# Optimization experiments

Measured on AMD Instinct MI355X. Metric: run time of the kernel, lower is better.

## Reference

```python
import jax, jax.numpy as jnp
import numpy as np

L, B, T, C, H, V, CTX = 4, 2, 1024, 1024, 16, 50257, 2048
D = C // H
EPS = 1e-5
NEG_SLOPE = 0.01


def layer_norm(x, w, b):
    mu = jnp.mean(x, axis=-1, keepdims=True)
    var = jnp.mean(jnp.square(x - mu), axis=-1, keepdims=True)
    return (x - mu) * jax.lax.rsqrt(var + EPS) * w + b


def setup_inputs() -> dict:
    key = jax.random.key(0)
    ks = jax.random.split(key, 8)
    s = 0.02  # init std as in _init_weights
    return {
        "idx": jax.random.randint(ks[0], (B, T), 0, V),
        "wte": jax.random.normal(ks[1], (V, C), jnp.float32) * s,
        "wpe": jax.random.normal(ks[2], (CTX, C), jnp.float32) * s,
        "ln1_w": jnp.ones((L, C), jnp.float32),
        "ln1_b": jnp.zeros((L, C), jnp.float32),
        "attn_w": jax.random.normal(ks[3], (L, C, 3 * C), jnp.float32) * s,
        "attn_b": jnp.zeros((L, 3 * C), jnp.float32),
        "proj_w": jax.random.normal(ks[4], (L, C, C), jnp.float32) * s,
        "proj_b": jnp.zeros((L, C), jnp.float32),
        "ln2_w": jnp.ones((L, C), jnp.float32),
        "ln2_b": jnp.zeros((L, C), jnp.float32),
        "fc_w": jax.random.normal(ks[5], (L, C, 4 * C), jnp.float32) * s,
        "fc_b": jnp.zeros((L, 4 * C), jnp.float32),
        "fcproj_w": jax.random.normal(ks[6], (L, 4 * C, C), jnp.float32) * s,
        "fcproj_b": jnp.zeros((L, C), jnp.float32),
        "lnf_w": jnp.ones((C,), jnp.float32),
        "lnf_b": jnp.zeros((C,), jnp.float32),
    }


def reference(idx, wte, wpe, ln1_w, ln1_b, attn_w, attn_b, proj_w, proj_b,
              ln2_w, ln2_b, fc_w, fc_b, fcproj_w, fcproj_b, lnf_w, lnf_b):
    t = idx.shape[1]
    x = wte[idx] + wpe[:t]  # [B,T,C]; dropout=0 => identity
    causal = jnp.tril(jnp.ones((t, t), bool))  # [T,T]
    scale = 1.0 / np.sqrt(D)
    for l in range(L):
        # --- causal self-attention ---
        h = layer_norm(x, ln1_w[l], ln1_b[l])
        qkv = h @ attn_w[l] + attn_b[l]  # [B,T,3C]
        q, k, v = jnp.split(qkv, 3, axis=-1)
        q = q.reshape(B, t, H, D)
        k = k.reshape(B, t, H, D)
        v = v.reshape(B, t, H, D)
        att = jnp.einsum('bthd,bshd->bhts', q, k) * scale  # [B,H,T,T]
        att = jnp.where(causal, att, -jnp.inf)
        att = jax.nn.softmax(att, axis=-1)
        y = jnp.einsum('bhts,bshd->bthd', att, v).reshape(B, t, C)
        x = x + y @ proj_w[l] + proj_b[l]
        # --- MLP ---
        h = layer_norm(x, ln2_w[l], ln2_b[l])
        h = h @ fc_w[l] + fc_b[l]
        h = jnp.where(h >= 0, h, NEG_SLOPE * h)  # LeakyReLU(0.01)
        x = x + h @ fcproj_w[l] + fcproj_b[l]
    x = layer_norm(x, lnf_w, lnf_b)
    # targets=None path: lm_head on last position only, tied weight = wte
    logits = x[:, -1:, :] @ wte.T  # [B,1,V]
    return logits
```

## Files before the change

### kernel.cpp

```cpp
#include <hip/hip_runtime.h>
#include <hip/hip_bf16.h>


#define TT 1024
#define CC 1024
#define NHEAD 16
#define DHEAD 64
#define NBATCH 2
#define VOCAB 50257

typedef __attribute__((ext_vector_type(8))) short bf16x8;
typedef __attribute__((ext_vector_type(4))) float f32x4;

#define GPTR(p) (const __attribute__((address_space(1))) void*)(p)
#define LPTR(p) (__attribute__((address_space(3))) void*)(p)

__device__ __forceinline__ unsigned short f2bf(float f) {
  union { float f; unsigned u; } v; v.f = f;
  unsigned r = v.u + 0x7fffu + ((v.u >> 16) & 1u);
  return (unsigned short)(r >> 16);
}
__device__ __forceinline__ float bf2f(unsigned short u) {
  union { unsigned u; float f; } v; v.u = ((unsigned)u) << 16;
  return v.f;
}

__device__ __forceinline__ f32x4 mfma_bf16(bf16x8 a, bf16x8 b, f32x4 c) {
  return __builtin_amdgcn_mfma_f32_16x16x32_bf16(a, b, c, 0, 0, 0);
}

__global__ __launch_bounds__(256) void embed_k(const int* __restrict__ idx,
    const float* __restrict__ wte, const float* __restrict__ wpe,
    float* __restrict__ x)
{
  int row = blockIdx.x;
  int t = row & (TT - 1);
  int tok = idx[row];
  const float4* a = (const float4*)(wte + (size_t)tok * CC);
  const float4* p = (const float4*)(wpe + (size_t)t * CC);
  float4* o = (float4*)(x + (size_t)row * CC);
  int i = threadIdx.x;
  float4 va = a[i], vp = p[i];
  o[i] = make_float4(va.x + vp.x, va.y + vp.y, va.z + vp.z, va.w + vp.w);
}

__device__ __forceinline__ unsigned pk2(float lo, float hi) {
  return (unsigned)f2bf(lo) | ((unsigned)f2bf(hi) << 16);
}

__global__ __launch_bounds__(256) void ln_k(const float* __restrict__ x,
    const float* __restrict__ w, const float* __restrict__ b,
    unsigned short* __restrict__ out)
{
  int row = blockIdx.x * 4 + (threadIdx.x >> 6);
  int lane = threadIdx.x & 63;
  const float* xr = x + (size_t)row * CC + lane * 16;
  float4 v[4];
  float s = 0.f, ss = 0.f;
#pragma unroll
  for (int i = 0; i < 4; ++i) {
    v[i] = *(const float4*)(xr + i * 4);
    s  += v[i].x + v[i].y + v[i].z + v[i].w;
    ss += v[i].x*v[i].x + v[i].y*v[i].y + v[i].z*v[i].z + v[i].w*v[i].w;
  }
#pragma unroll
  for (int off = 1; off < 64; off <<= 1) {
    s  += __shfl_xor(s, off, 64);
    ss += __shfl_xor(ss, off, 64);
  }
  float mu = s * (1.f / CC);
  float var = ss * (1.f / CC) - mu * mu;
  float rstd = rsqrtf(var + 1e-5f);
  const float* wr = w + lane * 16;
  const float* br = b + lane * 16;
  unsigned q[8];
#pragma unroll
  for (int i = 0; i < 4; ++i) {
    float4 wv = *(const float4*)(wr + i * 4);
    float4 bv = *(const float4*)(br + i * 4);
    float o0 = (v[i].x - mu) * rstd * wv.x + bv.x;
    float o1 = (v[i].y - mu) * rstd * wv.y + bv.y;
    float o2 = (v[i].z - mu) * rstd * wv.z + bv.z;
    float o3 = (v[i].w - mu) * rstd * wv.w + bv.w;
    q[i*2+0] = pk2(o0, o1);
    q[i*2+1] = pk2(o2, o3);
  }
  uint4* op = (uint4*)(out + (size_t)row * CC + lane * 16);
  op[0] = make_uint4(q[0], q[1], q[2], q[3]);
  op[1] = make_uint4(q[4], q[5], q[6], q[7]);
}

__global__ __launch_bounds__(256) void redln_k(float* __restrict__ x,
    const float* __restrict__ P, const float* __restrict__ bias,
    const float* __restrict__ lw, const float* __restrict__ lb,
    unsigned short* __restrict__ out, int splits)
{
  int row = blockIdx.x * 4 + (threadIdx.x >> 6);
  int lane = threadIdx.x & 63;
  const int c0 = lane * 16;
  float* xw = x + (size_t)row * CC + c0;
  float4 v[4];
#pragma unroll
  for (int i = 0; i < 4; ++i) v[i] = *(const float4*)(xw + i * 4);
  {
    const float4* b4 = (const float4*)(bias + c0);
#pragma unroll
    for (int i = 0; i < 4; ++i) {
      float4 bv = b4[i];
      v[i].x += bv.x; v[i].y += bv.y; v[i].z += bv.z; v[i].w += bv.w;
    }
  }
  for (int sp = 0; sp < splits; ++sp) {
    const float4* p4 = (const float4*)(P + ((size_t)sp * 2048 + row) * CC + c0);
#pragma unroll
    for (int i = 0; i < 4; ++i) {
      float4 pv = p4[i];
      v[i].x += pv.x; v[i].y += pv.y; v[i].z += pv.z; v[i].w += pv.w;
    }
  }
  float s = 0.f, ss = 0.f;
#pragma unroll
  for (int i = 0; i < 4; ++i) {
    *(float4*)(xw + i * 4) = v[i];
    s  += v[i].x + v[i].y + v[i].z + v[i].w;
    ss += v[i].x*v[i].x + v[i].y*v[i].y + v[i].z*v[i].z + v[i].w*v[i].w;
  }
#pragma unroll
  for (int off = 1; off < 64; off <<= 1) {
    s  += __shfl_xor(s, off, 64);
    ss += __shfl_xor(ss, off, 64);
  }
  float mu = s * (1.f / CC);
  float var = ss * (1.f / CC) - mu * mu;
  float rstd = rsqrtf(var + 1e-5f);
  const float* wr = lw + c0;
  const float* br = lb + c0;
  unsigned q[8];
#pragma unroll
  for (int i = 0; i < 4; ++i) {
    float4 wv = *(const float4*)(wr + i * 4);
    float4 bv = *(const float4*)(br + i * 4);
    float o0 = (v[i].x - mu) * rstd * wv.x + bv.x;
    float o1 = (v[i].y - mu) * rstd * wv.y + bv.y;
    float o2 = (v[i].z - mu) * rstd * wv.z + bv.z;
    float o3 = (v[i].w - mu) * rstd * wv.w + bv.w;
    q[i*2+0] = pk2(o0, o1);
    q[i*2+1] = pk2(o2, o3);
  }
  uint4* op = (uint4*)(out + (size_t)row * CC + c0);
  op[0] = make_uint4(q[0], q[1], q[2], q[3]);
  op[1] = make_uint4(q[4], q[5], q[6], q[7]);
}

__global__ void lnrow_k(const float* __restrict__ x,
    const float* __restrict__ w, const float* __restrict__ b,
    float* __restrict__ outv)
{
  int row = blockIdx.x;
  int lane = threadIdx.x;
  const float* xr = x + ((size_t)(row * TT + (TT - 1))) * CC + lane * 16;
  float4 v[4];
  float s = 0.f, ss = 0.f;
#pragma unroll
  for (int i = 0; i < 4; ++i) {
    v[i] = *(const float4*)(xr + i * 4);
    s  += v[i].x + v[i].y + v[i].z + v[i].w;
    ss += v[i].x*v[i].x + v[i].y*v[i].y + v[i].z*v[i].z + v[i].w*v[i].w;
  }
#pragma unroll
  for (int off = 1; off < 64; off <<= 1) {
    s  += __shfl_xor(s, off, 64);
    ss += __shfl_xor(ss, off, 64);
  }
  float mu = s * (1.f / CC);
  float var = ss * (1.f / CC) - mu * mu;
  float rstd = rsqrtf(var + 1e-5f);
  float* op = outv + (size_t)row * CC + lane * 16;
  const float* wr = w + lane * 16;
  const float* br = b + lane * 16;
#pragma unroll
  for (int i = 0; i < 4; ++i) {
    float4 wv = *(const float4*)(wr + i * 4);
    float4 bv = *(const float4*)(br + i * 4);
    float4 o;
    o.x = (v[i].x - mu) * rstd * wv.x + bv.x;
    o.y = (v[i].y - mu) * rstd * wv.y + bv.y;
    o.z = (v[i].z - mu) * rstd * wv.z + bv.z;
    o.w = (v[i].w - mu) * rstd * wv.w + bv.w;
    *(float4*)(op + i * 4) = o;
  }
}

__global__ __launch_bounds__(256) void wconv_k(const float* __restrict__ W,
    unsigned short* __restrict__ Wt, int K, int N)
{
  const size_t lo = (size_t)blockIdx.z * K * N;
  __shared__ float tile[64][65];
  const int k0 = blockIdx.x << 6;
  const int n0 = blockIdx.y << 6;
  const int t = threadIdx.x;
  {
    const int r = t >> 4, c4 = t & 15;
#pragma unroll
    for (int p = 0; p < 4; ++p) {
      int kr = r + (p << 4);
      float4 v = *(const float4*)(W + lo + (size_t)(k0 + kr) * N + n0 + (c4 << 2));
      tile[kr][(c4 << 2) + 0] = v.x;
      tile[kr][(c4 << 2) + 1] = v.y;
      tile[kr][(c4 << 2) + 2] = v.z;
      tile[kr][(c4 << 2) + 3] = v.w;
    }
  }
  __syncthreads();
  {
    const int n = t >> 2, kq = t & 3;
    bf16x8 o0, o1;
#pragma unroll
    for (int e = 0; e < 8; ++e) o0[e] = (short)f2bf(tile[(kq << 4) + e][n]);
#pragma unroll
    for (int e = 0; e < 8; ++e) o1[e] = (short)f2bf(tile[(kq << 4) + 8 + e][n]);
    unsigned short* dst = Wt + lo + (size_t)(n0 + n) * K + k0 + (kq << 4);
    *(bf16x8*)dst = o0;
    *(bf16x8*)(dst + 8) = o1;
  }
}

#define MODE_QKV  0
#define MODE_PART 1
#define MODE_FC   2

template<int MODE>
__global__ __launch_bounds__(256) void gemm_k(
    const unsigned short* __restrict__ A,
    const unsigned short* __restrict__ Wt,
    const float* __restrict__ bias,
    float* __restrict__ pbuf,
    unsigned short* __restrict__ obf,
    unsigned short* __restrict__ q_o,
    unsigned short* __restrict__ k_o,
    unsigned short* __restrict__ v_o,
    int M, int N, int K, int kchunk, int ncol0)
{
  __shared__ alignas(16) unsigned short Asm[2][128 * 64];
  __shared__ alignas(16) unsigned short Bsm[2][128 * 64];
  const int tid  = threadIdx.x;
  const int wave = tid >> 6, lane = tid & 63;
  const int lg = lane >> 4, ll = lane & 15;
  const int nTM = M >> 7, nTN = N >> 7;
  int bid = blockIdx.x;
  const int mt = bid % nTM; bid /= nTM;
  const int nt = bid % nTN;
  const int s  = bid / nTN;
  const int m0 = mt << 7, n0 = nt << 7;
  const int kb = s * kchunk;
  const int nIter = kchunk >> 6;
  const int wm = (wave >> 1) << 6, wn = (wave & 1) << 6;
  f32x4 acc[4][4] = {};

#define STAGE(BUF, K0)                                                        \
  {                                                                           \
    _Pragma("unroll")                                                         \
    for (int c = 0; c < 4; ++c) {                                             \
      const int seg = (wave << 2) + c;                                        \
      const int g = (seg << 6) + lane;                                        \
      const int row = g >> 3, kq = g & 7;                                     \
      const unsigned short* asrc = A  + (size_t)(m0 + row) * K + (K0) + (kq << 3); \
      const unsigned short* bsrc = Wt + (size_t)(n0 + row) * K + (K0) + (kq << 3); \
      __builtin_amdgcn_global_load_lds(GPTR(asrc), LPTR(&Asm[BUF][seg << 9]), 16, 0, 0); \
      __builtin_amdgcn_global_load_lds(GPTR(bsrc), LPTR(&Bsm[BUF][seg << 9]), 16, 0, 0); \
    }                                                                         \
  }

  STAGE(0, kb);
  if (nIter > 1) STAGE(1, kb + 64);

  for (int t = 0; t < nIter; ++t) {
    const int cur = t & 1;
    if (t + 1 < nIter) { asm volatile("s_waitcnt vmcnt(8)" ::: "memory"); }
    else               { asm volatile("s_waitcnt vmcnt(0)" ::: "memory"); }
    __builtin_amdgcn_sched_barrier(0);
    __builtin_amdgcn_s_barrier();

    const unsigned short* As = &Asm[cur][0];
    const unsigned short* Bs = &Bsm[cur][0];
#pragma unroll
    for (int kk = 0; kk < 2; ++kk) {
      bf16x8 af[4], bfr[4];
#pragma unroll
      for (int i = 0; i < 4; ++i)
        af[i] = *(const bf16x8*)(As + ((wm + i * 16 + ll) << 6) + (kk << 5) + (lg << 3));
#pragma unroll
      for (int j = 0; j < 4; ++j)
        bfr[j] = *(const bf16x8*)(Bs + ((wn + j * 16 + ll) << 6) + (kk << 5) + (lg << 3));
#pragma unroll
      for (int i = 0; i < 4; ++i)
#pragma unroll
        for (int j = 0; j < 4; ++j)
          acc[i][j] = mfma_bf16(af[i], bfr[j], acc[i][j]);
    }
    __builtin_amdgcn_sched_barrier(0);
    __builtin_amdgcn_s_barrier();
    if (t + 2 < nIter) STAGE(cur, kb + ((t + 2) << 6));
  }
#undef STAGE

#pragma unroll
  for (int j = 0; j < 4; ++j) {
    int gc = n0 + wn + j * 16 + ll;
    int gcol = ncol0 + gc;
    float bv = (MODE == MODE_PART) ? 0.f : bias[gcol];
#pragma unroll
    for (int i = 0; i < 4; ++i) {
      int gr0 = m0 + wm + i * 16 + (lg << 2);
#pragma unroll
      for (int r = 0; r < 4; ++r) {
        int grow = gr0 + r;
        float val = acc[i][j][r] + bv;
        if (MODE == MODE_QKV) {
          int which = gcol >> 10;
          int head = (gcol >> 6) & 15;
          int d = gcol & 63;
          int bb = grow >> 10, tt2 = grow & (TT - 1);
          unsigned short* dst = (which == 0) ? q_o : (which == 1) ? k_o : v_o;
          dst[(((size_t)((bb << 4) + head)) << 16) + ((size_t)tt2 << 6) + d] = f2bf(val);
        } else if (MODE == MODE_FC) {
          val = (val >= 0.f) ? val : 0.01f * val;
          obf[(size_t)grow * N + gc] = f2bf(val);
        } else {
          pbuf[((size_t)s * M + grow) * N + gc] = val;
        }
      }
    }
  }
}

__global__ __launch_bounds__(256) void attn_k(
    const unsigned short* __restrict__ Qb,
    const unsigned short* __restrict__ Kb,
    const unsigned short* __restrict__ Vb,
    unsigned short* __restrict__ ybuf)
{
  __shared__ alignas(16) unsigned short Ksm[64][72];
  __shared__ alignas(16) unsigned short Vtsm[64][64];
  __shared__ alignas(16) unsigned short Psm[4][16][72];
  const int tid = threadIdx.x;
  const int wave = tid >> 6, lane = tid & 63;
  const int lg = lane >> 4, ll = lane & 15;
  const int qt = blockIdx.x & 15, bh = blockIdx.x >> 4;
  const int b = bh >> 4, h = bh & 15;
  const size_t base = (size_t)bh << 16;
  const int q0 = qt << 6;
  const float SC = 0.125f * 1.44269504f;

  const int qrow = q0 + wave * 16 + ll;
  bf16x8 aq0 = *(const bf16x8*)(Qb + base + ((size_t)qrow << 6) + (lg << 3));
  bf16x8 aq1 = *(const bf16x8*)(Qb + base + ((size_t)qrow << 6) + 32 + (lg << 3));

  f32x4 accy[4] = {};
  float m_run[4], l_run[4];
#pragma unroll
  for (int r = 0; r < 4; ++r) { m_run[r] = -1e30f; l_run[r] = 0.f; }

  const int sk_row = tid >> 3, sk_cq = tid & 7;
  const int sv_d = tid & 63, sv_kq = tid >> 6;
  const int qg0 = q0 + wave * 16 + (lg << 2);

  for (int kb = 0; kb <= qt; ++kb) {
    const int kbase = kb << 6;
#pragma unroll
    for (int p = 0; p < 2; ++p) {
      int r = sk_row + (p << 5);
      bf16x8 kv = *(const bf16x8*)(Kb + base + ((size_t)(kbase + r) << 6) + (sk_cq << 3));
      *(bf16x8*)&Ksm[r][sk_cq << 3] = kv;
    }
#pragma unroll
    for (int p = 0; p < 2; ++p) {
      int kq8 = sv_kq + (p << 2);
      bf16x8 wv;
#pragma unroll
      for (int e = 0; e < 8; ++e)
        wv[e] = (short)Vb[base + ((size_t)(kbase + (kq8 << 3) + e) << 6) + sv_d];
      int u = kq8 ^ (sv_d & 7);
      *(bf16x8*)&Vtsm[sv_d][u << 3] = wv;
    }
    __syncthreads();

    float p_[4][4];
    float rmax[4] = {-1e30f, -1e30f, -1e30f, -1e30f};
#pragma unroll
    for (int kk = 0; kk < 4; ++kk) {
      f32x4 z = {};
      bf16x8 bk0 = *(const bf16x8*)&Ksm[kk * 16 + ll][lg << 3];
      bf16x8 bk1 = *(const bf16x8*)&Ksm[kk * 16 + ll][32 + (lg << 3)];
      z = mfma_bf16(aq0, bk0, z);
      z = mfma_bf16(aq1, bk1, z);
      int key = kbase + kk * 16 + ll;
#pragma unroll
      for (int r = 0; r < 4; ++r) {
        float v = z[r] * SC;
        v = (key > qg0 + r) ? -1e30f : v;
        p_[kk][r] = v;
        rmax[r] = fmaxf(rmax[r], v);
      }
    }
#pragma unroll
    for (int off = 1; off < 16; off <<= 1)
#pragma unroll
      for (int r = 0; r < 4; ++r)
        rmax[r] = fmaxf(rmax[r], __shfl_xor(rmax[r], off, 64));

    float alpha[4], rsum[4];
#pragma unroll
    for (int r = 0; r < 4; ++r) {
      float mn = fmaxf(m_run[r], rmax[r]);
      alpha[r] = exp2f(m_run[r] - mn);
      m_run[r] = mn;
      rsum[r] = 0.f;
    }
#pragma unroll
    for (int kk = 0; kk < 4; ++kk)
#pragma unroll
      for (int r = 0; r < 4; ++r) {
        float e = exp2f(p_[kk][r] - m_run[r]);
        p_[kk][r] = e;
        rsum[r] += e;
      }
#pragma unroll
    for (int off = 1; off < 16; off <<= 1)
#pragma unroll
      for (int r = 0; r < 4; ++r)
        rsum[r] += __shfl_xor(rsum[r], off, 64);
#pragma unroll
    for (int r = 0; r < 4; ++r)
      l_run[r] = l_run[r] * alpha[r] + rsum[r];
#pragma unroll
    for (int df = 0; df < 4; ++df)
#pragma unroll
      for (int r = 0; r < 4; ++r)
        accy[df][r] *= alpha[r];

#pragma unroll
    for (int kk = 0; kk < 4; ++kk)
#pragma unroll
      for (int r = 0; r < 4; ++r)
        Psm[wave][(lg << 2) + r][kk * 16 + ll] = f2bf(p_[kk][r]);
    bf16x8 pa0 = *(const bf16x8*)&Psm[wave][ll][lg << 3];
    bf16x8 pa1 = *(const bf16x8*)&Psm[wave][ll][32 + (lg << 3)];

#pragma unroll
    for (int df = 0; df < 4; ++df) {
      int d = df * 16 + ll;
      int u0 = lg ^ (d & 7);
      int u1 = (4 + lg) ^ (d & 7);
      bf16x8 bv0 = *(const bf16x8*)&Vtsm[d][u0 << 3];
      bf16x8 bv1 = *(const bf16x8*)&Vtsm[d][u1 << 3];
      accy[df] = mfma_bf16(pa0, bv0, accy[df]);
      accy[df] = mfma_bf16(pa1, bv1, accy[df]);
    }
    __syncthreads();
  }

#pragma unroll
  for (int df = 0; df < 4; ++df)
#pragma unroll
    for (int r = 0; r < 4; ++r) {
      int qr = qg0 + r;
      float y = accy[df][r] / l_run[r];
      ybuf[(((size_t)((b << 10) + qr)) << 10) + (h << 6) + df * 16 + ll] = f2bf(y);
    }
}

__global__ __launch_bounds__(256) void gemv_k(const float* __restrict__ W,
    int ldw, const float* __restrict__ xv, int K,
    float* __restrict__ part, int N)
{
  __shared__ float xs[2][128];
  const int tid = threadIdx.x;
  const int n = blockIdx.x * 256 + tid;
  const int ks = blockIdx.y;
  if (tid < 128) xs[0][tid] = xv[ks * 128 + tid];
  else           xs[1][tid - 128] = xv[K + ks * 128 + (tid - 128)];
  __syncthreads();
  float a0 = 0.f, a1 = 0.f;
  const float* wp = W + (size_t)(ks * 128) * ldw + n;
#pragma unroll 4
  for (int k = 0; k < 128; ++k) {
    float w = wp[(size_t)k * ldw];
    a0 += xs[0][k] * w;
    a1 += xs[1][k] * w;
  }
  part[((size_t)ks * 2 + 0) * N + n] = a0;
  part[((size_t)ks * 2 + 1) * N + n] = a1;
}

#define MG_PLAIN 0
#define MG_LEAKY 1
#define MG_ADDX  2
template<int MG>
__global__ __launch_bounds__(256) void gmerge_k(const float* __restrict__ part,
    const float* __restrict__ bias, float* __restrict__ outp, int N, int KT)
{
  int n = blockIdx.x * 256 + threadIdx.x;
#pragma unroll
  for (int b = 0; b < 2; ++b) {
    float s = bias[n];
    for (int ks = 0; ks < KT; ++ks)
      s += part[((size_t)ks * 2 + b) * N + n];
    if (MG == MG_PLAIN) outp[(size_t)b * N + n] = s;
    else if (MG == MG_LEAKY) outp[(size_t)b * N + n] = (s >= 0.f) ? s : 0.01f * s;
    else outp[((size_t)(b * TT + TT - 1)) * CC + n] += s;
  }
}

__global__ __launch_bounds__(256) void attnlast_k(
    const float* __restrict__ q_last,
    const unsigned short* __restrict__ Kb,
    const unsigned short* __restrict__ Vb,
    float* __restrict__ apart)
{
  __shared__ float qs[64];
  __shared__ float wm[4], wl[4], wacc[4][64];
  const int tid = threadIdx.x;
  const int wave = tid >> 6, lane = tid & 63;
  const int bh = blockIdx.x, ks = blockIdx.y;
  const int b = bh >> 4, h = bh & 15;
  const size_t base = (size_t)bh << 16;
  const int key = ks * 256 + wave * 64 + lane;

  if (tid < 64) qs[tid] = q_last[b * CC + h * 64 + tid];
  __syncthreads();

  float s = 0.f;
  const unsigned short* kp = Kb + base + ((size_t)key << 6);
#pragma unroll
  for (int o = 0; o < 8; ++o) {
    bf16x8 kv = *(const bf16x8*)(kp + (o << 3));
#pragma unroll
    for (int e = 0; e < 8; ++e)
      s += qs[(o << 3) + e] * bf2f((unsigned short)kv[e]);
  }
  s *= 0.125f;
  float m = s;
#pragma unroll
  for (int off = 1; off < 64; off <<= 1)
    m = fmaxf(m, __shfl_xor(m, off, 64));
  float p = __expf(s - m);
  float l = p;
#pragma unroll
  for (int off = 1; off < 64; off <<= 1)
    l += __shfl_xor(l, off, 64);

  float acc = 0.f;
  const unsigned short* vp = Vb + base + ((size_t)(ks * 256 + wave * 64) << 6);
  for (int j = 0; j < 64; ++j) {
    float pj = __shfl(p, j, 64);
    acc += pj * bf2f(vp[((size_t)j << 6) + lane]);
  }
  if (lane == 0) { wm[wave] = m; wl[wave] = l; }
  wacc[wave][lane] = acc;
  __syncthreads();
  if (wave == 0) {
    float m0 = fmaxf(fmaxf(wm[0], wm[1]), fmaxf(wm[2], wm[3]));
    float lt = 0.f, at = 0.f;
#pragma unroll
    for (int sI = 0; sI < 4; ++sI) {
      float f = __expf(wm[sI] - m0);
      lt += wl[sI] * f;
      at += wacc[sI][lane] * f;
    }
    float* op = apart + ((size_t)bh * 4 + ks) * 66;
    if (lane == 0) { op[0] = m0; op[1] = lt; }
    op[2 + lane] = at;
  }
}

__global__ void attnmerge_k(const float* __restrict__ apart,
    float* __restrict__ y_last)
{
  const int bh = blockIdx.x, lane = threadIdx.x;
  const int b = bh >> 4, h = bh & 15;
  const float* p0 = apart + (size_t)bh * 4 * 66;
  float m0 = fmaxf(fmaxf(p0[0], p0[66]), fmaxf(p0[132], p0[198]));
  float lt = 0.f, at = 0.f;
#pragma unroll
  for (int s = 0; s < 4; ++s) {
    const float* ps = p0 + s * 66;
    float f = __expf(ps[0] - m0);
    lt += ps[1] * f;
    at += ps[2 + lane] * f;
  }
  y_last[b * CC + h * 64 + lane] = at / lt;
}

__global__ __launch_bounds__(256) void head_k(const float* __restrict__ xf,
    const float* __restrict__ wte, float* __restrict__ out)
{
  int v = (blockIdx.x << 2) + (threadIdx.x >> 6);
  if (v >= VOCAB) return;
  int lane = threadIdx.x & 63;
  const float4* wr = (const float4*)(wte + (size_t)v * CC);
  const float4* x0 = (const float4*)xf;
  const float4* x1 = (const float4*)(xf + CC);
  float a0 = 0.f, a1 = 0.f;
#pragma unroll
  for (int i = 0; i < 4; ++i) {
    float4 wv = wr[lane + i * 64];
    float4 p0 = x0[lane + i * 64];
    float4 p1 = x1[lane + i * 64];
    a0 += wv.x * p0.x + wv.y * p0.y + wv.z * p0.z + wv.w * p0.w;
    a1 += wv.x * p1.x + wv.y * p1.y + wv.z * p1.z + wv.w * p1.w;
  }
#pragma unroll
  for (int off = 1; off < 64; off <<= 1) {
    a0 += __shfl_xor(a0, off, 64);
    a1 += __shfl_xor(a1, off, 64);
  }
  if (lane == 0) {
    out[v] = a0;
    out[VOCAB + v] = a1;
  }
}

extern "C" void kernel_launch(void* const* d_in, const int* in_sizes, int n_in,
                              void* d_out, int out_size, void* d_ws, size_t ws_size,
                              hipStream_t stream)
{
  const int*   idx      = (const int*)d_in[0];
  const float* wte      = (const float*)d_in[1];
  const float* wpe      = (const float*)d_in[2];
  const float* ln1_w    = (const float*)d_in[3];
  const float* ln1_b    = (const float*)d_in[4];
  const float* attn_w   = (const float*)d_in[5];
  const float* attn_b   = (const float*)d_in[6];
  const float* proj_w   = (const float*)d_in[7];
  const float* proj_b   = (const float*)d_in[8];
  const float* ln2_w    = (const float*)d_in[9];
  const float* ln2_b    = (const float*)d_in[10];
  const float* fc_w     = (const float*)d_in[11];
  const float* fc_b     = (const float*)d_in[12];
  const float* fcproj_w = (const float*)d_in[13];
  const float* fcproj_b = (const float*)d_in[14];
  const float* lnf_w    = (const float*)d_in[15];
  const float* lnf_b    = (const float*)d_in[16];
  float* out = (float*)d_out;

  const size_t MB = 1u << 20;
  char* ws = (char*)d_ws;
  float*          x   = (float*)ws;
  unsigned short* h   = (unsigned short*)(ws + 8*MB);
  unsigned short* qb  = (unsigned short*)(ws + 12*MB);
  unsigned short* kb_ = (unsigned short*)(ws + 16*MB);
  unsigned short* vb  = (unsigned short*)(ws + 20*MB);
  unsigned short* yb  = (unsigned short*)(ws + 24*MB);
  unsigned short* hf  = (unsigned short*)(ws + 28*MB);
  char* sm = ws + 44*MB;
  float* xf     = (float*)(sm + 0);
  float* xs1    = (float*)(sm + 16*1024);
  float* xs2    = (float*)(sm + 32*1024);
  float* ylast  = (float*)(sm + 48*1024);
  float* qlast  = (float*)(sm + 64*1024);
  float* hlast  = (float*)(sm + 80*1024);
  float* gpart  = (float*)(sm + 128*1024);
  float* apart  = (float*)(sm + 512*1024);
  unsigned short* wt_attn   = (unsigned short*)(ws + 46*MB);
  unsigned short* wt_proj   = (unsigned short*)(ws + 70*MB);
  unsigned short* wt_fc     = (unsigned short*)(ws + 76*MB);
  unsigned short* wt_fcproj = (unsigned short*)(ws + 100*MB);
  float*          Ppart     = (float*)(ws + 124*MB);

  embed_k<<<NBATCH * TT, 256, 0, stream>>>(idx, wte, wpe, x);

  wconv_k<<<dim3(16, 48, 4), 256, 0, stream>>>(attn_w, wt_attn, 1024, 3072);
  wconv_k<<<dim3(16, 16, 3), 256, 0, stream>>>(proj_w, wt_proj, 1024, 1024);
  wconv_k<<<dim3(16, 64, 3), 256, 0, stream>>>(fc_w, wt_fc, 1024, 4096);
  wconv_k<<<dim3(64, 16, 3), 256, 0, stream>>>(fcproj_w, wt_fcproj, 4096, 1024);

  ln_k<<<512, 256, 0, stream>>>(x, ln1_w, ln1_b, h);

  for (int l = 0; l < 3; ++l) {
    gemm_k<MODE_QKV><<<16 * 24, 256, 0, stream>>>(h,
        wt_attn + (size_t)l * 3072 * 1024, attn_b + (size_t)l * 3 * CC,
        nullptr, nullptr, qb, kb_, vb, 2048, 3072, 1024, 1024, 0);
    attn_k<<<NBATCH * NHEAD * 16, 256, 0, stream>>>(qb, kb_, vb, yb);
    gemm_k<MODE_PART><<<16 * 8 * 4, 256, 0, stream>>>(yb,
        wt_proj + (size_t)l * 1024 * 1024, nullptr,
        Ppart, nullptr, nullptr, nullptr, nullptr, 2048, 1024, 1024, 256, 0);
    redln_k<<<512, 256, 0, stream>>>(x, Ppart, proj_b + l * CC,
        ln2_w + l * CC, ln2_b + l * CC, h, 4);
    gemm_k<MODE_FC><<<16 * 32, 256, 0, stream>>>(h,
        wt_fc + (size_t)l * 1024 * 4096, fc_b + (size_t)l * 4 * CC,
        nullptr, hf, nullptr, nullptr, nullptr, 2048, 4096, 1024, 1024, 0);
    gemm_k<MODE_PART><<<16 * 8 * 4, 256, 0, stream>>>(hf,
        wt_fcproj + (size_t)l * 4096 * 1024, nullptr,
        Ppart, nullptr, nullptr, nullptr, nullptr, 2048, 1024, 4096, 1024, 0);
    redln_k<<<512, 256, 0, stream>>>(x, Ppart, fcproj_b + l * CC,
        ln1_w + (l + 1) * CC, ln1_b + (l + 1) * CC, h, 4);
  }

  {
    const int l = 3;
    gemm_k<MODE_QKV><<<16 * 16, 256, 0, stream>>>(h,
        wt_attn + (size_t)l * 3072 * 1024 + (size_t)1024 * 1024,
        attn_b + (size_t)l * 3 * CC,
        nullptr, nullptr, qb, kb_, vb, 2048, 2048, 1024, 1024, 1024);
    lnrow_k<<<2, 64, 0, stream>>>(x, ln1_w + l * CC, ln1_b + l * CC, xs1);
    gemv_k<<<dim3(4, 8), 256, 0, stream>>>(attn_w + (size_t)l * CC * 3 * CC,
        3072, xs1, 1024, gpart, 1024);
    gmerge_k<MG_PLAIN><<<4, 256, 0, stream>>>(gpart, attn_b + (size_t)l * 3 * CC,
        qlast, 1024, 8);
    attnlast_k<<<dim3(32, 4), 256, 0, stream>>>(qlast, kb_, vb, apart);
    attnmerge_k<<<32, 64, 0, stream>>>(apart, ylast);
    gemv_k<<<dim3(4, 8), 256, 0, stream>>>(proj_w + (size_t)l * CC * CC,
        1024, ylast, 1024, gpart, 1024);
    gmerge_k<MG_ADDX><<<4, 256, 0, stream>>>(gpart, proj_b + l * CC, x, 1024, 8);
    lnrow_k<<<2, 64, 0, stream>>>(x, ln2_w + l * CC, ln2_b + l * CC, xs2);
    gemv_k<<<dim3(16, 8), 256, 0, stream>>>(fc_w + (size_t)l * CC * 4 * CC,
        4096, xs2, 1024, gpart, 4096);
    gmerge_k<MG_LEAKY><<<16, 256, 0, stream>>>(gpart, fc_b + (size_t)l * 4 * CC,
        hlast, 4096, 8);
    gemv_k<<<dim3(4, 32), 256, 0, stream>>>(fcproj_w + (size_t)l * 4 * CC * CC,
        1024, hlast, 4096, gpart, 1024);
    gmerge_k<MG_ADDX><<<4, 256, 0, stream>>>(gpart, fcproj_b + l * CC, x, 1024, 32);
  }

  lnrow_k<<<2, 64, 0, stream>>>(x, lnf_w, lnf_b, xf);
  head_k<<<(VOCAB + 3) / 4, 256, 0, stream>>>(xf, wte, out);
}
```

Baseline: 727.0 us.

## Fuse embed+LN, merge weight conversions, remap GEMM blocks per XCD, fuse last-layer tail

Merges the embedding and first layernorm into a single kernel and folds the four weight-conversion launches into one. GEMM block IDs are remapped so contiguous tiles land on the same XCD. The last-layer single-row tail is rebuilt from fewer, fused kernels: q GEMV reading bf16 h, single-pass online-softmax attention, proj GEMV that adds the bias and residual directly, LN2 fused into the fc GEMV, and a final merge fused with the final layernorm. This cuts launch count and intermediate traffic, but the tail GEMVs now run on very few blocks with long serial K loops, so each launch may be slower.

Result: slower. 814.8 us (+12.1%).

```diff
diff --git a/kernel.cpp b/kernel.cpp
--- a/kernel.cpp
+++ b/kernel.cpp
@@ -29,50 +29,92 @@
   return __builtin_amdgcn_mfma_f32_16x16x32_bf16(a, b, c, 0, 0, 0);
 }
 
-__global__ __launch_bounds__(256) void embed_k(const int* __restrict__ idx,
-    const float* __restrict__ wte, const float* __restrict__ wpe,
-    float* __restrict__ x)
-{
-  int row = blockIdx.x;
-  int t = row & (TT - 1);
-  int tok = idx[row];
-  const float4* a = (const float4*)(wte + (size_t)tok * CC);
-  const float4* p = (const float4*)(wpe + (size_t)t * CC);
-  float4* o = (float4*)(x + (size_t)row * CC);
-  int i = threadIdx.x;
-  float4 va = a[i], vp = p[i];
-  o[i] = make_float4(va.x + vp.x, va.y + vp.y, va.z + vp.z, va.w + vp.w);
-}
-
 __device__ __forceinline__ unsigned pk2(float lo, float hi) {
   return (unsigned)f2bf(lo) | ((unsigned)f2bf(hi) << 16);
 }
 
-__global__ __launch_bounds__(256) void ln_k(const float* __restrict__ x,
-    const float* __restrict__ w, const float* __restrict__ b,
-    unsigned short* __restrict__ out)
-{
-  int row = blockIdx.x * 4 + (threadIdx.x >> 6);
-  int lane = threadIdx.x & 63;
-  const float* xr = x + (size_t)row * CC + lane * 16;
-  float4 v[4];
-  float s = 0.f, ss = 0.f;
-#pragma unroll
-  for (int i = 0; i < 4; ++i) {
-    v[i] = *(const float4*)(xr + i * 4);
-    s  += v[i].x + v[i].y + v[i].z + v[i].w;
-    ss += v[i].x*v[i].x + v[i].y*v[i].y + v[i].z*v[i].z + v[i].w*v[i].w;
-  }
+__global__ __launch_bounds__(256) void embedln_k(const int* __restrict__ idx,
+    const float* __restrict__ wte, const float* __restrict__ wpe,
+    const float* __restrict__ lw, const float* __restrict__ lb,
+    float* __restrict__ x, unsigned short* __restrict__ h)
+{
+  __shared__ float rs[4], rss[4];
+  const int row = blockIdx.x;
+  const int t = row & (TT - 1);
+  const int tok = idx[row];
+  const int tid = threadIdx.x, wave = tid >> 6, lane = tid & 63;
+  float4 va = ((const float4*)(wte + (size_t)tok * CC))[tid];
+  float4 vp = ((const float4*)(wpe + (size_t)t * CC))[tid];
+  float4 v = make_float4(va.x + vp.x, va.y + vp.y, va.z + vp.z, va.w + vp.w);
+  ((float4*)(x + (size_t)row * CC))[tid] = v;
+  float s  = v.x + v.y + v.z + v.w;
+  float ss = v.x*v.x + v.y*v.y + v.z*v.z + v.w*v.w;
 #pragma unroll
   for (int off = 1; off < 64; off <<= 1) {
     s  += __shfl_xor(s, off, 64);
     ss += __shfl_xor(ss, off, 64);
   }
+  if (lane == 0) { rs[wave] = s; rss[wave] = ss; }
+  __syncthreads();
+  s  = rs[0] + rs[1] + rs[2] + rs[3];
+  ss = rss[0] + rss[1] + rss[2] + rss[3];
   float mu = s * (1.f / CC);
   float var = ss * (1.f / CC) - mu * mu;
   float rstd = rsqrtf(var + 1e-5f);
-  const float* wr = w + lane * 16;
-  const float* br = b + lane * 16;
+  float4 wv = ((const float4*)lw)[tid];
+  float4 bv = ((const float4*)lb)[tid];
+  float o0 = (v.x - mu) * rstd * wv.x + bv.x;
+  float o1 = (v.y - mu) * rstd * wv.y + bv.y;
+  float o2 = (v.z - mu) * rstd * wv.z + bv.z;
+  float o3 = (v.w - mu) * rstd * wv.w + bv.w;
+  ((uint2*)(h + (size_t)row * CC))[tid] = make_uint2(pk2(o0, o1), pk2(o2, o3));
+}
+
+__global__ __launch_bounds__(256) void redln_k(float* __restrict__ x,
+    const float* __restrict__ P, const float* __restrict__ bias,
+    const float* __restrict__ lw, const float* __restrict__ lb,
+    unsigned short* __restrict__ out, int splits)
+{
+  int row = blockIdx.x * 4 + (threadIdx.x >> 6);
+  int lane = threadIdx.x & 63;
+  const int c0 = lane * 16;
+  float* xw = x + (size_t)row * CC + c0;
+  float4 v[4];
+#pragma unroll
+  for (int i = 0; i < 4; ++i) v[i] = *(const float4*)(xw + i * 4);
+  {
+    const float4* b4 = (const float4*)(bias + c0);
+#pragma unroll
+    for (int i = 0; i < 4; ++i) {
+      float4 bv = b4[i];
+      v[i].x += bv.x; v[i].y += bv.y; v[i].z += bv.z; v[i].w += bv.w;
+    }
+  }
+  for (int sp = 0; sp < splits; ++sp) {
+    const float4* p4 = (const float4*)(P + ((size_t)sp * 2048 + row) * CC + c0);
+#pragma unroll
+    for (int i = 0; i < 4; ++i) {
+      float4 pv = p4[i];
+      v[i].x += pv.x; v[i].y += pv.y; v[i].z += pv.z; v[i].w += pv.w;
+    }
+  }
+  float s = 0.f, ss = 0.f;
+#pragma unroll
+  for (int i = 0; i < 4; ++i) {
+    *(float4*)(xw + i * 4) = v[i];
+    s  += v[i].x + v[i].y + v[i].z + v[i].w;
+    ss += v[i].x*v[i].x + v[i].y*v[i].y + v[i].z*v[i].z + v[i].w*v[i].w;
+  }
+#pragma unroll
+  for (int off = 1; off < 64; off <<= 1) {
+    s  += __shfl_xor(s, off, 64);
+    ss += __shfl_xor(ss, off, 64);
+  }
+  float mu = s * (1.f / CC);
+  float var = ss * (1.f / CC) - mu * mu;
+  float rstd = rsqrtf(var + 1e-5f);
+  const float* wr = lw + c0;
+  const float* br = lb + c0;
   unsigned q[8];
 #pragma unroll
   for (int i = 0; i < 4; ++i) {
@@ -85,126 +127,49 @@
     q[i*2+0] = pk2(o0, o1);
     q[i*2+1] = pk2(o2, o3);
   }
-  uint4* op = (uint4*)(out + (size_t)row * CC + lane * 16);
-  op[0] = make_uint4(q[0], q[1], q[2], q[3]);
-  op[1] = make_uint4(q[4], q[5], q[6], q[7]);
-}
-
-__global__ __launch_bounds__(256) void redln_k(float* __restrict__ x,
-    const float* __restrict__ P, const float* __restrict__ bias,
-    const float* __restrict__ lw, const float* __restrict__ lb,
-    unsigned short* __restrict__ out, int splits)
-{
-  int row = blockIdx.x * 4 + (threadIdx.x >> 6);
-  int lane = threadIdx.x & 63;
-  const int c0 = lane * 16;
-  float* xw = x + (size_t)row * CC + c0;
-  float4 v[4];
-#pragma unroll
-  for (int i = 0; i < 4; ++i) v[i] = *(const float4*)(xw + i * 4);
-  {
-    const float4* b4 = (const float4*)(bias + c0);
-#pragma unroll
-    for (int i = 0; i < 4; ++i) {
-      float4 bv = b4[i];
-      v[i].x += bv.x; v[i].y += bv.y; v[i].z += bv.z; v[i].w += bv.w;
-    }
-  }
-  for (int sp = 0; sp < splits; ++sp) {
-    const float4* p4 = (const float4*)(P + ((size_t)sp * 2048 + row) * CC + c0);
-#pragma unroll
-    for (int i = 0; i < 4; ++i) {
-      float4 pv = p4[i];
-      v[i].x += pv.x; v[i].y += pv.y; v[i].z += pv.z; v[i].w += pv.w;
-    }
-  }
-  float s = 0.f, ss = 0.f;
-#pragma unroll
-  for (int i = 0; i < 4; ++i) {
-    *(float4*)(xw + i * 4) = v[i];
-    s  += v[i].x + v[i].y + v[i].z + v[i].w;
-    ss += v[i].x*v[i].x + v[i].y*v[i].y + v[i].z*v[i].z + v[i].w*v[i].w;
-  }
-#pragma unroll
-  for (int off = 1; off < 64; off <<= 1) {
-    s  += __shfl_xor(s, off, 64);
-    ss += __shfl_xor(ss, off, 64);
-  }
-  float mu = s * (1.f / CC);
-  float var = ss * (1.f / CC) - mu * mu;
-  float rstd = rsqrtf(var + 1e-5f);
-  const float* wr = lw + c0;
-  const float* br = lb + c0;
-  unsigned q[8];
-#pragma unroll
-  for (int i = 0; i < 4; ++i) {
-    float4 wv = *(const float4*)(wr + i * 4);
-    float4 bv = *(const float4*)(br + i * 4);
-    float o0 = (v[i].x - mu) * rstd * wv.x + bv.x;
-    float o1 = (v[i].y - mu) * rstd * wv.y + bv.y;
-    float o2 = (v[i].z - mu) * rstd * wv.z + bv.z;
-    float o3 = (v[i].w - mu) * rstd * wv.w + bv.w;
-    q[i*2+0] = pk2(o0, o1);
-    q[i*2+1] = pk2(o2, o3);
-  }
   uint4* op = (uint4*)(out + (size_t)row * CC + c0);
   op[0] = make_uint4(q[0], q[1], q[2], q[3]);
   op[1] = make_uint4(q[4], q[5], q[6], q[7]);
 }
 
-__global__ void lnrow_k(const float* __restrict__ x,
-    const float* __restrict__ w, const float* __restrict__ b,
-    float* __restrict__ outv)
-{
-  int row = blockIdx.x;
-  int lane = threadIdx.x;
-  const float* xr = x + ((size_t)(row * TT + (TT - 1))) * CC + lane * 16;
-  float4 v[4];
-  float s = 0.f, ss = 0.f;
-#pragma unroll
-  for (int i = 0; i < 4; ++i) {
-    v[i] = *(const float4*)(xr + i * 4);
-    s  += v[i].x + v[i].y + v[i].z + v[i].w;
-    ss += v[i].x*v[i].x + v[i].y*v[i].y + v[i].z*v[i].z + v[i].w*v[i].w;
-  }
-#pragma unroll
-  for (int off = 1; off < 64; off <<= 1) {
-    s  += __shfl_xor(s, off, 64);
-    ss += __shfl_xor(ss, off, 64);
-  }
-  float mu = s * (1.f / CC);
-  float var = ss * (1.f / CC) - mu * mu;
-  float rstd = rsqrtf(var + 1e-5f);
-  float* op = outv + (size_t)row * CC + lane * 16;
-  const float* wr = w + lane * 16;
-  const float* br = b + lane * 16;
-#pragma unroll
-  for (int i = 0; i < 4; ++i) {
-    float4 wv = *(const float4*)(wr + i * 4);
-    float4 bv = *(const float4*)(br + i * 4);
-    float4 o;
-    o.x = (v[i].x - mu) * rstd * wv.x + bv.x;
-    o.y = (v[i].y - mu) * rstd * wv.y + bv.y;
-    o.z = (v[i].z - mu) * rstd * wv.z + bv.z;
-    o.w = (v[i].w - mu) * rstd * wv.w + bv.w;
-    *(float4*)(op + i * 4) = o;
-  }
-}
-
-__global__ __launch_bounds__(256) void wconv_k(const float* __restrict__ W,
-    unsigned short* __restrict__ Wt, int K, int N)
-{
-  const size_t lo = (size_t)blockIdx.z * K * N;
+__global__ __launch_bounds__(256) void wconv_all_k(
+    const float* __restrict__ attn_w, unsigned short* __restrict__ wt_attn,
+    const float* __restrict__ proj_w, unsigned short* __restrict__ wt_proj,
+    const float* __restrict__ fc_w,   unsigned short* __restrict__ wt_fc,
+    const float* __restrict__ fcp_w,  unsigned short* __restrict__ wt_fcp)
+{
+  int b = blockIdx.x;
+  const float* W; unsigned short* Wt; int K, N, kx, ny;
+  if (b < 3072) {
+    int layer = b / 768, tI = b % 768;
+    K = 1024; N = 3072;
+    W = attn_w + (size_t)layer * K * N; Wt = wt_attn + (size_t)layer * K * N;
+    kx = tI % 16; ny = tI / 16;
+  } else if (b < 3840) {
+    b -= 3072; int layer = b / 256, tI = b % 256;
+    K = 1024; N = 1024;
+    W = proj_w + (size_t)layer * K * N; Wt = wt_proj + (size_t)layer * K * N;
+    kx = tI % 16; ny = tI / 16;
+  } else if (b < 6912) {
+    b -= 3840; int layer = b / 1024, tI = b % 1024;
+    K = 1024; N = 4096;
+    W = fc_w + (size_t)layer * K * N; Wt = wt_fc + (size_t)layer * K * N;
+    kx = tI % 16; ny = tI / 16;
+  } else {
+    b -= 6912; int layer = b / 1024, tI = b % 1024;
+    K = 4096; N = 1024;
+    W = fcp_w + (size_t)layer * K * N; Wt = wt_fcp + (size_t)layer * K * N;
+    kx = tI % 64; ny = tI / 64;
+  }
   __shared__ float tile[64][65];
-  const int k0 = blockIdx.x << 6;
-  const int n0 = blockIdx.y << 6;
+  const int k0 = kx << 6, n0 = ny << 6;
   const int t = threadIdx.x;
   {
     const int r = t >> 4, c4 = t & 15;
 #pragma unroll
     for (int p = 0; p < 4; ++p) {
       int kr = r + (p << 4);
-      float4 v = *(const float4*)(W + lo + (size_t)(k0 + kr) * N + n0 + (c4 << 2));
+      float4 v = *(const float4*)(W + (size_t)(k0 + kr) * N + n0 + (c4 << 2));
       tile[kr][(c4 << 2) + 0] = v.x;
       tile[kr][(c4 << 2) + 1] = v.y;
       tile[kr][(c4 << 2) + 2] = v.z;
@@ -219,7 +184,7 @@
     for (int e = 0; e < 8; ++e) o0[e] = (short)f2bf(tile[(kq << 4) + e][n]);
 #pragma unroll
     for (int e = 0; e < 8; ++e) o1[e] = (short)f2bf(tile[(kq << 4) + 8 + e][n]);
-    unsigned short* dst = Wt + lo + (size_t)(n0 + n) * K + k0 + (kq << 4);
+    unsigned short* dst = Wt + (size_t)(n0 + n) * K + k0 + (kq << 4);
     *(bf16x8*)dst = o0;
     *(bf16x8*)(dst + 8) = o1;
   }
@@ -247,7 +212,13 @@
   const int wave = tid >> 6, lane = tid & 63;
   const int lg = lane >> 4, ll = lane & 15;
   const int nTM = M >> 7, nTN = N >> 7;
-  int bid = blockIdx.x;
+  int bid;
+  {
+    const int nwg = gridDim.x;
+    const int q = nwg >> 3, r = nwg & 7;
+    const int xcd = blockIdx.x & 7, idxw = blockIdx.x >> 3;
+    bid = (xcd < r ? xcd * (q + 1) : r * (q + 1) + (xcd - r) * q) + idxw;
+  }
   const int mt = bid % nTM; bid /= nTM;
   const int nt = bid % nTN;
   const int s  = bid / nTN;
@@ -470,93 +441,87 @@
     }
 }
 
-__global__ __launch_bounds__(256) void gemv_k(const float* __restrict__ W,
-    int ldw, const float* __restrict__ xv, int K,
-    float* __restrict__ part, int N)
-{
-  __shared__ float xs[2][128];
+
+__global__ __launch_bounds__(256) void qlast_k(
+    const unsigned short* __restrict__ hbuf,
+    const float* __restrict__ Wq, const float* __restrict__ bq,
+    float* __restrict__ qlast)
+{
+  __shared__ float xs[2][1024];
   const int tid = threadIdx.x;
+  {
+    const int b = tid >> 7, c0 = (tid & 127) << 3;
+    bf16x8 hv = *(const bf16x8*)(hbuf + ((size_t)(b * TT + TT - 1)) * CC + c0);
+#pragma unroll
+    for (int e = 0; e < 8; ++e) xs[b][c0 + e] = bf2f((unsigned short)hv[e]);
+  }
+  __syncthreads();
   const int n = blockIdx.x * 256 + tid;
-  const int ks = blockIdx.y;
-  if (tid < 128) xs[0][tid] = xv[ks * 128 + tid];
-  else           xs[1][tid - 128] = xv[K + ks * 128 + (tid - 128)];
-  __syncthreads();
   float a0 = 0.f, a1 = 0.f;
-  const float* wp = W + (size_t)(ks * 128) * ldw + n;
-#pragma unroll 4
-  for (int k = 0; k < 128; ++k) {
-    float w = wp[(size_t)k * ldw];
-    a0 += xs[0][k] * w;
-    a1 += xs[1][k] * w;
-  }
-  part[((size_t)ks * 2 + 0) * N + n] = a0;
-  part[((size_t)ks * 2 + 1) * N + n] = a1;
-}
-
-#define MG_PLAIN 0
-#define MG_LEAKY 1
-#define MG_ADDX  2
-template<int MG>
-__global__ __launch_bounds__(256) void gmerge_k(const float* __restrict__ part,
-    const float* __restrict__ bias, float* __restrict__ outp, int N, int KT)
-{
-  int n = blockIdx.x * 256 + threadIdx.x;
-#pragma unroll
-  for (int b = 0; b < 2; ++b) {
-    float s = bias[n];
-    for (int ks = 0; ks < KT; ++ks)
-      s += part[((size_t)ks * 2 + b) * N + n];
-    if (MG == MG_PLAIN) outp[(size_t)b * N + n] = s;
-    else if (MG == MG_LEAKY) outp[(size_t)b * N + n] = (s >= 0.f) ? s : 0.01f * s;
-    else outp[((size_t)(b * TT + TT - 1)) * CC + n] += s;
-  }
-}
-
-__global__ __launch_bounds__(256) void attnlast_k(
+  const float* wp = Wq + n;
+  for (int k = 0; k < 1024; k += 8)
+#pragma unroll
+    for (int u = 0; u < 8; ++u) {
+      float w = wp[(size_t)(k + u) * 3072];
+      a0 += xs[0][k + u] * w;
+      a1 += xs[1][k + u] * w;
+    }
+  float bb = bq[n];
+  qlast[n] = a0 + bb;
+  qlast[1024 + n] = a1 + bb;
+}
+
+__global__ __launch_bounds__(256) void attnlast2_k(
     const float* __restrict__ q_last,
     const unsigned short* __restrict__ Kb,
     const unsigned short* __restrict__ Vb,
-    float* __restrict__ apart)
+    float* __restrict__ y_last)
 {
   __shared__ float qs[64];
   __shared__ float wm[4], wl[4], wacc[4][64];
   const int tid = threadIdx.x;
   const int wave = tid >> 6, lane = tid & 63;
-  const int bh = blockIdx.x, ks = blockIdx.y;
+  const int bh = blockIdx.x;
   const int b = bh >> 4, h = bh & 15;
   const size_t base = (size_t)bh << 16;
-  const int key = ks * 256 + wave * 64 + lane;
-
   if (tid < 64) qs[tid] = q_last[b * CC + h * 64 + tid];
   __syncthreads();
 
-  float s = 0.f;
-  const unsigned short* kp = Kb + base + ((size_t)key << 6);
-#pragma unroll
-  for (int o = 0; o < 8; ++o) {
-    bf16x8 kv = *(const bf16x8*)(kp + (o << 3));
-#pragma unroll
-    for (int e = 0; e < 8; ++e)
-      s += qs[(o << 3) + e] * bf2f((unsigned short)kv[e]);
-  }
-  s *= 0.125f;
-  float m = s;
-#pragma unroll
-  for (int off = 1; off < 64; off <<= 1)
-    m = fmaxf(m, __shfl_xor(m, off, 64));
-  float p = __expf(s - m);
-  float l = p;
-#pragma unroll
-  for (int off = 1; off < 64; off <<= 1)
-    l += __shfl_xor(l, off, 64);
-
-  float acc = 0.f;
-  const unsigned short* vp = Vb + base + ((size_t)(ks * 256 + wave * 64) << 6);
-  for (int j = 0; j < 64; ++j) {
-    float pj = __shfl(p, j, 64);
-    acc += pj * bf2f(vp[((size_t)j << 6) + lane]);
-  }
-  if (lane == 0) { wm[wave] = m; wl[wave] = l; }
+  float m_w = -1e30f, l_w = 0.f, acc = 0.f;
+  for (int ks = 0; ks < 4; ++ks) {
+    const int key = ks * 256 + wave * 64 + lane;
+    float s = 0.f;
+    const unsigned short* kp = Kb + base + ((size_t)key << 6);
+#pragma unroll
+    for (int o = 0; o < 8; ++o) {
+      bf16x8 kv = *(const bf16x8*)(kp + (o << 3));
+#pragma unroll
+      for (int e = 0; e < 8; ++e)
+        s += qs[(o << 3) + e] * bf2f((unsigned short)kv[e]);
+    }
+    s *= 0.125f;
+    float m = s;
+#pragma unroll
+    for (int off = 1; off < 64; off <<= 1)
+      m = fmaxf(m, __shfl_xor(m, off, 64));
+    float mn = fmaxf(m_w, m);
+    float alpha = __expf(m_w - mn);
+    m_w = mn;
+    float p = __expf(s - mn);
+    float ps = p;
+#pragma unroll
+    for (int off = 1; off < 64; off <<= 1)
+      ps += __shfl_xor(ps, off, 64);
+    l_w = l_w * alpha + ps;
+    float a2 = 0.f;
+    const unsigned short* vp = Vb + base + ((size_t)(ks * 256 + wave * 64) << 6);
+    for (int j = 0; j < 64; ++j) {
+      float pj = __shfl(p, j, 64);
+      a2 += pj * bf2f(vp[((size_t)j << 6) + lane]);
+    }
+    acc = acc * alpha + a2;
+  }
+  if (lane == 0) { wm[wave] = m_w; wl[wave] = l_w; }
   wacc[wave][lane] = acc;
   __syncthreads();
   if (wave == 0) {
@@ -568,28 +533,173 @@
       lt += wl[sI] * f;
       at += wacc[sI][lane] * f;
     }
-    float* op = apart + ((size_t)bh * 4 + ks) * 66;
-    if (lane == 0) { op[0] = m0; op[1] = lt; }
-    op[2 + lane] = at;
-  }
-}
-
-__global__ void attnmerge_k(const float* __restrict__ apart,
-    float* __restrict__ y_last)
-{
-  const int bh = blockIdx.x, lane = threadIdx.x;
-  const int b = bh >> 4, h = bh & 15;
-  const float* p0 = apart + (size_t)bh * 4 * 66;
-  float m0 = fmaxf(fmaxf(p0[0], p0[66]), fmaxf(p0[132], p0[198]));
-  float lt = 0.f, at = 0.f;
-#pragma unroll
-  for (int s = 0; s < 4; ++s) {
-    const float* ps = p0 + s * 66;
-    float f = __expf(ps[0] - m0);
-    lt += ps[1] * f;
-    at += ps[2 + lane] * f;
-  }
-  y_last[b * CC + h * 64 + lane] = at / lt;
+    y_last[b * CC + h * 64 + lane] = at / lt;
+  }
+}
+
+__global__ __launch_bounds__(256) void projlast_k(
+    const float* __restrict__ ylast,
+    const float* __restrict__ W, const float* __restrict__ bias,
+    float* __restrict__ x)
+{
+  __shared__ float ys[2][1024];
+  const int tid = threadIdx.x;
+#pragma unroll
+  for (int i = 0; i < 8; ++i) {
+    int c = tid * 8 + i;
+    ys[c >> 10][c & 1023] = ylast[c];
+  }
+  __syncthreads();
+  const int n = blockIdx.x * 256 + tid;
+  float a0 = 0.f, a1 = 0.f;
+  const float* wp = W + n;
+  for (int k = 0; k < 1024; k += 8)
+#pragma unroll
+    for (int u = 0; u < 8; ++u) {
+      float w = wp[(size_t)(k + u) * 1024];
+      a0 += ys[0][k + u] * w;
+      a1 += ys[1][k + u] * w;
+    }
+  float bb = bias[n];
+  x[((size_t)(TT - 1)) * CC + n]          += a0 + bb;
+  x[((size_t)(2 * TT - 1)) * CC + n]      += a1 + bb;
+}
+
+__global__ __launch_bounds__(256) void fclast_k(
+    const float* __restrict__ x,
+    const float* __restrict__ lw, const float* __restrict__ lb,
+    const float* __restrict__ W, const float* __restrict__ bias,
+    float* __restrict__ hlast)
+{
+  __shared__ float xs[2][1024];
+  const int tid = threadIdx.x;
+  const int wave = tid >> 6, lane = tid & 63;
+  if (wave < 2) {
+    const float* xr = x + ((size_t)(wave * TT + TT - 1)) * CC + lane * 16;
+    float4 v[4];
+    float s = 0.f, ss = 0.f;
+#pragma unroll
+    for (int i = 0; i < 4; ++i) {
+      v[i] = *(const float4*)(xr + i * 4);
+      s  += v[i].x + v[i].y + v[i].z + v[i].w;
+      ss += v[i].x*v[i].x + v[i].y*v[i].y + v[i].z*v[i].z + v[i].w*v[i].w;
+    }
+#pragma unroll
+    for (int off = 1; off < 64; off <<= 1) {
+      s  += __shfl_xor(s, off, 64);
+      ss += __shfl_xor(ss, off, 64);
+    }
+    float mu = s * (1.f / CC);
+    float var = ss * (1.f / CC) - mu * mu;
+    float rstd = rsqrtf(var + 1e-5f);
+    const float* wr = lw + lane * 16;
+    const float* br = lb + lane * 16;
+#pragma unroll
+    for (int i = 0; i < 4; ++i) {
+      float4 wv = *(const float4*)(wr + i * 4);
+      float4 bv = *(const float4*)(br + i * 4);
+      xs[wave][lane * 16 + i * 4 + 0] = (v[i].x - mu) * rstd * wv.x + bv.x;
+      xs[wave][lane * 16 + i * 4 + 1] = (v[i].y - mu) * rstd * wv.y + bv.y;
+      xs[wave][lane * 16 + i * 4 + 2] = (v[i].z - mu) * rstd * wv.z + bv.z;
+      xs[wave][lane * 16 + i * 4 + 3] = (v[i].w - mu) * rstd * wv.w + bv.w;
+    }
+  }
+  __syncthreads();
+  const int n = blockIdx.x * 256 + tid;
+  float a0 = 0.f, a1 = 0.f;
+  const float* wp = W + n;
+  for (int k = 0; k < 1024; k += 8)
+#pragma unroll
+    for (int u = 0; u < 8; ++u) {
+      float w = wp[(size_t)(k + u) * 4096];
+      a0 += xs[0][k + u] * w;
+      a1 += xs[1][k + u] * w;
+    }
+  float bb = bias[n];
+  a0 += bb; a1 += bb;
+  hlast[n]        = (a0 >= 0.f) ? a0 : 0.01f * a0;
+  hlast[4096 + n] = (a1 >= 0.f) ? a1 : 0.01f * a1;
+}
+
+__global__ __launch_bounds__(256) void fcprojpart_k(
+    const float* __restrict__ hlast,
+    const float* __restrict__ W,
+    float* __restrict__ part)
+{
+  __shared__ float hs[2][1024];
+  const int tid = threadIdx.x;
+  const int ks = blockIdx.y;
+#pragma unroll
+  for (int i = 0; i < 8; ++i) {
+    int c = tid * 8 + i;
+    hs[c >> 10][c & 1023] = hlast[(size_t)(c >> 10) * 4096 + ks * 1024 + (c & 1023)];
+  }
+  __syncthreads();
+  const int n = blockIdx.x * 256 + tid;
+  float a0 = 0.f, a1 = 0.f;
+  const float* wp = W + (size_t)(ks * 1024) * 1024 + n;
+  for (int k = 0; k < 1024; k += 8)
+#pragma unroll
+    for (int u = 0; u < 8; ++u) {
+      float w = wp[(size_t)(k + u) * 1024];
+      a0 += hs[0][k + u] * w;
+      a1 += hs[1][k + u] * w;
+    }
+  part[(size_t)(ks * 2 + 0) * 1024 + n] = a0;
+  part[(size_t)(ks * 2 + 1) * 1024 + n] = a1;
+}
+
+__global__ void lnfmerge_k(const float* __restrict__ x,
+    const float* __restrict__ part, const float* __restrict__ bias,
+    const float* __restrict__ lw, const float* __restrict__ lb,
+    float* __restrict__ xf)
+{
+  const int row = blockIdx.x;
+  const int lane = threadIdx.x;
+  const int c0 = lane * 16;
+  const float* xr = x + ((size_t)(row * TT + TT - 1)) * CC + c0;
+  float4 v[4];
+  float s = 0.f, ss = 0.f;
+#pragma unroll
+  for (int i = 0; i < 4; ++i) {
+    v[i] = *(const float4*)(xr + i * 4);
+    float4 bv = *(const float4*)(bias + c0 + i * 4);
+    v[i].x += bv.x; v[i].y += bv.y; v[i].z += bv.z; v[i].w += bv.w;
+  }
+#pragma unroll
+  for (int ks = 0; ks < 4; ++ks) {
+    const float* pp = part + (size_t)(ks * 2 + row) * 1024 + c0;
+#pragma unroll
+    for (int i = 0; i < 4; ++i) {
+      float4 pv = *(const float4*)(pp + i * 4);
+      v[i].x += pv.x; v[i].y += pv.y; v[i].z += pv.z; v[i].w += pv.w;
+    }
+  }
+#pragma unroll
+  for (int i = 0; i < 4; ++i) {
+    s  += v[i].x + v[i].y + v[i].z + v[i].w;
+    ss += v[i].x*v[i].x + v[i].y*v[i].y + v[i].z*v[i].z + v[i].w*v[i].w;
+  }
+#pragma unroll
+  for (int off = 1; off < 64; off <<= 1) {
+    s  += __shfl_xor(s, off, 64);
+    ss += __shfl_xor(ss, off, 64);
+  }
+  float mu = s * (1.f / CC);
+  float var = ss * (1.f / CC) - mu * mu;
+  float rstd = rsqrtf(var + 1e-5f);
+  float* op = xf + (size_t)row * CC + c0;
+#pragma unroll
+  for (int i = 0; i < 4; ++i) {
+    float4 wv = *(const float4*)(lw + c0 + i * 4);
+    float4 bv = *(const float4*)(lb + c0 + i * 4);
+    float4 o;
+    o.x = (v[i].x - mu) * rstd * wv.x + bv.x;
+    o.y = (v[i].y - mu) * rstd * wv.y + bv.y;
+    o.z = (v[i].z - mu) * rstd * wv.z + bv.z;
+    o.w = (v[i].w - mu) * rstd * wv.w + bv.w;
+    *(float4*)(op + i * 4) = o;
+  }
 }
 
 __global__ __launch_bounds__(256) void head_k(const float* __restrict__ xf,
@@ -655,27 +765,20 @@
   unsigned short* hf  = (unsigned short*)(ws + 28*MB);
   char* sm = ws + 44*MB;
   float* xf     = (float*)(sm + 0);
-  float* xs1    = (float*)(sm + 16*1024);
-  float* xs2    = (float*)(sm + 32*1024);
   float* ylast  = (float*)(sm + 48*1024);
   float* qlast  = (float*)(sm + 64*1024);
   float* hlast  = (float*)(sm + 80*1024);
   float* gpart  = (float*)(sm + 128*1024);
-  float* apart  = (float*)(sm + 512*1024);
   unsigned short* wt_attn   = (unsigned short*)(ws + 46*MB);
   unsigned short* wt_proj   = (unsigned short*)(ws + 70*MB);
   unsigned short* wt_fc     = (unsigned short*)(ws + 76*MB);
   unsigned short* wt_fcproj = (unsigned short*)(ws + 100*MB);
   float*          Ppart     = (float*)(ws + 124*MB);
 
-  embed_k<<<NBATCH * TT, 256, 0, stream>>>(idx, wte, wpe, x);
-
-  wconv_k<<<dim3(16, 48, 4), 256, 0, stream>>>(attn_w, wt_attn, 1024, 3072);
-  wconv_k<<<dim3(16, 16, 3), 256, 0, stream>>>(proj_w, wt_proj, 1024, 1024);
-  wconv_k<<<dim3(16, 64, 3), 256, 0, stream>>>(fc_w, wt_fc, 1024, 4096);
-  wconv_k<<<dim3(64, 16, 3), 256, 0, stream>>>(fcproj_w, wt_fcproj, 4096, 1024);
-
-  ln_k<<<512, 256, 0, stream>>>(x, ln1_w, ln1_b, h);
+  embedln_k<<<NBATCH * TT, 256, 0, stream>>>(idx, wte, wpe, ln1_w, ln1_b, x, h);
+
+  wconv_all_k<<<9984, 256, 0, stream>>>(attn_w, wt_attn, proj_w, wt_proj,
+                                        fc_w, wt_fc, fcproj_w, wt_fcproj);
 
   for (int l = 0; l < 3; ++l) {
     gemm_k<MODE_QKV><<<16 * 24, 256, 0, stream>>>(h,
@@ -703,26 +806,18 @@
         wt_attn + (size_t)l * 3072 * 1024 + (size_t)1024 * 1024,
         attn_b + (size_t)l * 3 * CC,
         nullptr, nullptr, qb, kb_, vb, 2048, 2048, 1024, 1024, 1024);
-    lnrow_k<<<2, 64, 0, stream>>>(x, ln1_w + l * CC, ln1_b + l * CC, xs1);
-    gemv_k<<<dim3(4, 8), 256, 0, stream>>>(attn_w + (size_t)l * CC * 3 * CC,
-        3072, xs1, 1024, gpart, 1024);
-    gmerge_k<MG_PLAIN><<<4, 256, 0, stream>>>(gpart, attn_b + (size_t)l * 3 * CC,
-        qlast, 1024, 8);
-    attnlast_k<<<dim3(32, 4), 256, 0, stream>>>(qlast, kb_, vb, apart);
-    attnmerge_k<<<32, 64, 0, stream>>>(apart, ylast);
-    gemv_k<<<dim3(4, 8), 256, 0, stream>>>(proj_w + (size_t)l * CC * CC,
-        1024, ylast, 1024, gpart, 1024);
-    gmerge_k<MG_ADDX><<<4, 256, 0, stream>>>(gpart, proj_b + l * CC, x, 1024, 8);
-    lnrow_k<<<2, 64, 0, stream>>>(x, ln2_w + l * CC, ln2_b + l * CC, xs2);
-    gemv_k<<<dim3(16, 8), 256, 0, stream>>>(fc_w + (size_t)l * CC * 4 * CC,
-        4096, xs2, 1024, gpart, 4096);
-    gmerge_k<MG_LEAKY><<<16, 256, 0, stream>>>(gpart, fc_b + (size_t)l * 4 * CC,
-        hlast, 4096, 8);
-    gemv_k<<<dim3(4, 32), 256, 0, stream>>>(fcproj_w + (size_t)l * 4 * CC * CC,
-        1024, hlast, 4096, gpart, 1024);
-    gmerge_k<MG_ADDX><<<4, 256, 0, stream>>>(gpart, fcproj_b + l * CC, x, 1024, 32);
-  }
-
-  lnrow_k<<<2, 64, 0, stream>>>(x, lnf_w, lnf_b, xf);
+    qlast_k<<<4, 256, 0, stream>>>(h, attn_w + (size_t)l * CC * 3 * CC,
+        attn_b + (size_t)l * 3 * CC, qlast);
+    attnlast2_k<<<32, 256, 0, stream>>>(qlast, kb_, vb, ylast);
+    projlast_k<<<4, 256, 0, stream>>>(ylast, proj_w + (size_t)l * CC * CC,
+        proj_b + l * CC, x);
+    fclast_k<<<16, 256, 0, stream>>>(x, ln2_w + l * CC, ln2_b + l * CC,
+        fc_w + (size_t)l * CC * 4 * CC, fc_b + (size_t)l * 4 * CC, hlast);
+    fcprojpart_k<<<dim3(4, 4), 256, 0, stream>>>(hlast,
+        fcproj_w + (size_t)l * 4 * CC * CC, gpart);
+    lnfmerge_k<<<2, 64, 0, stream>>>(x, gpart, fcproj_b + l * CC,
+        lnf_w, lnf_b, xf);
+  }
+
   head_k<<<(VOCAB + 3) / 4, 256, 0, stream>>>(xf, wte, out);
 }
```
